# Optimization experiments

Measured on AMD Instinct MI355X. Metric: run time of the kernel, lower is better.

Reference implementation:

```python
import jax, jax.numpy as jnp
import numpy as np

NUM_HEADS = 16
EMBED = 1024
BLOCK = 2048
VOCAB = 32000
HEAD = EMBED // NUM_HEADS


def setup_inputs() -> dict:
    key = jax.random.key(0)
    ks = jax.random.split(key, 9)
    B, T = 2, 2048
    x = jax.random.randint(ks[0], (B, T), 0, VOCAB)
    target = jax.random.randint(ks[1], (B, T), 0, VOCAB)
    s = 0.02
    tok_emb = jax.random.normal(ks[2], (VOCAB, EMBED), jnp.float32) * s
    pos_emb = jax.random.normal(ks[3], (BLOCK, EMBED), jnp.float32) * s
    Wq = jax.random.normal(ks[4], (EMBED, EMBED), jnp.float32) * s
    Wk = jax.random.normal(ks[5], (EMBED, EMBED), jnp.float32) * s
    Wv = jax.random.normal(ks[6], (EMBED, EMBED), jnp.float32) * s
    W_lm = jax.random.normal(ks[7], (EMBED, VOCAB), jnp.float32) * s
    b_lm = jnp.zeros((VOCAB,), jnp.float32)
    return {"x": x, "target": target, "tok_emb": tok_emb, "pos_emb": pos_emb,
            "Wq": Wq, "Wk": Wk, "Wv": Wv, "W_lm": W_lm, "b_lm": b_lm}


def reference(x, target, tok_emb, pos_emb, Wq, Wk, Wv, W_lm, b_lm):
    B, T = x.shape
    h = tok_emb[x] + pos_emb[:T]                       # [B,T,E]
    # fused QKV projections, then split into heads (equivalent to per-head Linears + concat)
    q = (h @ Wq).reshape(B, T, NUM_HEADS, HEAD)
    k = (h @ Wk).reshape(B, T, NUM_HEADS, HEAD)
    v = (h @ Wv).reshape(B, T, NUM_HEADS, HEAD)
    scores = jnp.einsum("bqhd,bkhd->bhqk", q, k) / (HEAD ** 0.5)
    causal = jnp.tril(jnp.ones((T, T), bool))
    scores = jnp.where(causal, scores, -jnp.inf)
    attn = jax.nn.softmax(scores, axis=-1)             # [B,H,T,T]
    out = jnp.einsum("bhqk,bkhd->bqhd", attn, v).reshape(B, T, EMBED)
    logits = out @ W_lm + b_lm                         # [B,T,V]
    logits_flat = logits.reshape(B * T, VOCAB)
    logp = jax.nn.log_softmax(logits_flat, axis=-1)
    loss = -jnp.take_along_axis(logp, target.reshape(-1, 1), axis=-1).mean()
    return logits_flat, loss
```

## Files before the change

kernel.cpp:

```cpp
#include <hip/hip_runtime.h>
#include <cstdint>
#include <cstddef>

#define EMB   1024
#define TSEQ  2048
#define NBATCH 2
#define NHEAD 16
#define HDIM  64
#define VOCAB 32000
#define ROWS  4096
#define NCB   125

typedef __attribute__((ext_vector_type(8))) short short8;
typedef __attribute__((ext_vector_type(4))) float f32x4;

__device__ __forceinline__ unsigned short f2bf(float f) {
  unsigned int u = __float_as_uint(f);
  u = (u + 0x7FFFu + ((u >> 16) & 1u)) >> 16;
  return (unsigned short)u;
}

__device__ __forceinline__ void gload16(const void* g, void* l) {
  typedef __attribute__((address_space(1))) const unsigned int gu;
  typedef __attribute__((address_space(3))) unsigned int lu;
  __builtin_amdgcn_global_load_lds((gu*)g, (lu*)l, 16, 0, 0);
}

__global__ void convT(const float* __restrict__ in, unsigned short* __restrict__ out,
                      int R, int C) {
  __shared__ float tile[32][33];
  const int ct = blockIdx.x, rt = blockIdx.y;
  const int t = threadIdx.x;
  const int r0 = t >> 5;
  const int c  = t & 31;
#pragma unroll
  for (int i = 0; i < 4; ++i) {
    int r = r0 + i * 8;
    tile[r][c] = in[(size_t)(rt * 32 + r) * C + ct * 32 + c];
  }
  __syncthreads();
#pragma unroll
  for (int i = 0; i < 4; ++i) {
    int r = r0 + i * 8;
    out[(size_t)(ct * 32 + r) * R + rt * 32 + c] = f2bf(tile[c][r]);
  }
}

__global__ void embed_kernel(const int* __restrict__ x, const float* __restrict__ tok,
                             const float* __restrict__ pos, unsigned short* __restrict__ h) {
  const int idx = blockIdx.x * 256 + threadIdx.x;
  const int row = idx >> 8;
  const int c4  = idx & 255;
  const int tpos = row & (TSEQ - 1);
  const int token = x[row];
  float4 a = *(const float4*)(tok + (size_t)token * EMB + c4 * 4);
  float4 p = *(const float4*)(pos + (size_t)tpos * EMB + c4 * 4);
  unsigned int lo = (unsigned int)f2bf(a.x + p.x) | ((unsigned int)f2bf(a.y + p.y) << 16);
  unsigned int hi = (unsigned int)f2bf(a.z + p.z) | ((unsigned int)f2bf(a.w + p.w) << 16);
  *(uint2*)(h + (size_t)idx * 4) = make_uint2(lo, hi);
}

template <int EPI>
__global__ void gemm_bt(const unsigned short* __restrict__ A,
                        const unsigned short* __restrict__ Bt,
                        void* __restrict__ Cout,
                        float scale, int M, int N, int K) {
  __shared__ unsigned short As[2][128 * 32];
  __shared__ unsigned short Bs[2][128 * 32];
  const int t  = threadIdx.x;
  const int l  = t & 63;
  const int w  = t >> 6;
  const int wr = w >> 1, wc = w & 1;
  const int m0 = blockIdx.y * 128;
  const int n0 = blockIdx.x * 128;
  const int KT = K >> 5;

  f32x4 acc[4][4] = {};

  const int crow = t >> 2;
  const int coff = (t & 3) * 16;
  const size_t abase = ((size_t)(m0 + crow) * K) * 2 + coff;
  const size_t bbase = ((size_t)(n0 + crow) * K) * 2 + coff;
  const size_t rstep = (size_t)64 * K * 2;
  const char* Ab = (const char*)A;
  const char* Bb = (const char*)Bt;

#define STAGE(buf, kt_) do {                                              \
    size_t ko = (size_t)(kt_) * 64;                                       \
    gload16(Ab + abase + ko,         (char*)&As[(buf)][0] + t * 16);      \
    gload16(Ab + abase + rstep + ko, (char*)&As[(buf)][0] + t * 16 + 4096);\
    gload16(Bb + bbase + ko,         (char*)&Bs[(buf)][0] + t * 16);      \
    gload16(Bb + bbase + rstep + ko, (char*)&Bs[(buf)][0] + t * 16 + 4096);\
  } while (0)

  const int lr  = l & 15;
  const int lkb = (l >> 4) * 16;

#define COMPUTE(buf) do {                                                  \
    const char* ab = (const char*)&As[(buf)][0];                           \
    const char* bb = (const char*)&Bs[(buf)][0];                           \
    short8 fa[4], fb[4];                                                   \
    _Pragma("unroll")                                                      \
    for (int m = 0; m < 4; ++m)                                            \
      fa[m] = *(const short8*)(ab + (wr * 64 + m * 16 + lr) * 64 + lkb);   \
    _Pragma("unroll")                                                      \
    for (int n = 0; n < 4; ++n)                                            \
      fb[n] = *(const short8*)(bb + (wc * 64 + n * 16 + lr) * 64 + lkb);   \
    _Pragma("unroll")                                                      \
    for (int m = 0; m < 4; ++m)                                            \
      _Pragma("unroll")                                                    \
      for (int n = 0; n < 4; ++n)                                          \
        acc[m][n] = __builtin_amdgcn_mfma_f32_16x16x32_bf16(               \
            fa[m], fb[n], acc[m][n], 0, 0, 0);                             \
  } while (0)

  STAGE(0, 0);
  __syncthreads();
  int cur = 0;
  for (int kt = 0; kt < KT; ++kt) {
    if (kt + 1 < KT) STAGE(cur ^ 1, kt + 1);
    COMPUTE(cur);
    __syncthreads();
    cur ^= 1;
  }
#undef STAGE
#undef COMPUTE

  const int orow = m0 + wr * 64 + (l >> 4) * 4;
  const int ocol = n0 + wc * 64 + lr;
#pragma unroll
  for (int m = 0; m < 4; ++m) {
#pragma unroll
    for (int n = 0; n < 4; ++n) {
      const int col = ocol + n * 16;
      if (EPI == 1) {
        unsigned short* C = (unsigned short*)Cout;
#pragma unroll
        for (int r = 0; r < 4; ++r) {
          int row = orow + m * 16 + r;
          C[(size_t)row * N + col] = f2bf(acc[m][n][r] * scale);
        }
      } else {
        unsigned short* C = (unsigned short*)Cout;
        int row0 = orow + m * 16;
        int bb_ = row0 >> 11, tq = row0 & 2047;
        int hh = col >> 6, dd = col & 63;
        unsigned int lo = (unsigned int)f2bf(acc[m][n][0]) | ((unsigned int)f2bf(acc[m][n][1]) << 16);
        unsigned int hi = (unsigned int)f2bf(acc[m][n][2]) | ((unsigned int)f2bf(acc[m][n][3]) << 16);
        *(uint2*)&C[(((size_t)(bb_ * NHEAD + hh) * HDIM + dd) * TSEQ) + tq] = make_uint2(lo, hi);
      }
    }
  }
}

__global__ __launch_bounds__(256)
void attn_mfma(const unsigned short* __restrict__ Qbf,
               const unsigned short* __restrict__ Kbf,
               const unsigned short* __restrict__ Vtbf,
               unsigned short* __restrict__ Obf) {
  const int qt = (gridDim.x - 1) - blockIdx.x;
  const int h  = blockIdx.y;
  const int b  = blockIdx.z;
  const int t  = threadIdx.x, w = t >> 6, l = t & 63;
  const int g  = l >> 4, c = l & 15;
  const int qw = qt * 64 + w * 16;
  const int qg = qw + c;

  __shared__ unsigned short Ks[2][32 * 64];
  __shared__ unsigned short Vs[2][64 * 32];

  const unsigned short* Qrow = Qbf + ((size_t)(b * TSEQ + qg) * EMB + h * HDIM);
  short8 qfrag[2];
  qfrag[0] = *(const short8*)(Qrow + g * 8);
  qfrag[1] = *(const short8*)(Qrow + g * 8 + 32);

  f32x4 accO[4] = {};
  float mrun = -3e38f, lsum = 0.0f;

  const int kvt = t >> 3, kch = t & 7;
  const char* Kg = (const char*)(Kbf + ((size_t)(b * TSEQ + kvt) * EMB + h * HDIM))
                   + (((kch * 16) ^ ((kvt & 7) << 4)));
  const int dt = t >> 2, vch = t & 3;
  const char* Vg = (const char*)(Vtbf + (((size_t)(b * NHEAD + h) * HDIM + dt) * TSEQ))
                   + vch * 16;
  const size_t kstep = (size_t)32 * EMB * 2;
  const size_t vstep = (size_t)32 * 2;

#define ASTAGE(buf, kt_) do {                                               \
    gload16(Kg + (size_t)(kt_) * kstep, (char*)&Ks[buf][0] + t * 16);       \
    gload16(Vg + (size_t)(kt_) * vstep, (char*)&Vs[buf][0] + t * 16);       \
  } while (0)

  const int nkt = 2 * qt + 2;
  ASTAGE(0, 0);
  __syncthreads();
  int cur = 0;
  for (int kt = 0; kt < nkt; ++kt) {
    if (kt + 1 < nkt) ASTAGE(cur ^ 1, kt + 1);
    const int k0 = kt * 32;

    const char* kb = (const char*)&Ks[cur][0];
    f32x4 sa[2] = {};
#pragma unroll
    for (int kc = 0; kc < 2; ++kc) {
#pragma unroll
      for (int kh = 0; kh < 2; ++kh) {
        short8 ka = *(const short8*)(kb + (kc * 16 + c) * 128 +
                                     ((g * 16 + kh * 64) ^ ((c & 7) << 4)));
        sa[kc] = __builtin_amdgcn_mfma_f32_16x16x32_bf16(ka, qfrag[kh], sa[kc], 0, 0, 0);
      }
    }

    float sv[8];
#pragma unroll
    for (int kc = 0; kc < 2; ++kc)
#pragma unroll
      for (int r = 0; r < 4; ++r) {
        int kv = k0 + kc * 16 + g * 4 + r;
        sv[kc * 4 + r] = (kv > qg) ? -3e38f : sa[kc][r];
      }
    float pm = sv[0];
#pragma unroll
    for (int i = 1; i < 8; ++i) pm = fmaxf(pm, sv[i]);
    pm = fmaxf(pm, __shfl_xor(pm, 16));
    pm = fmaxf(pm, __shfl_xor(pm, 32));
    const float mnew = fmaxf(mrun, pm);
    const float alpha = __expf(mrun - mnew);
    float ps = 0.0f;
#pragma unroll
    for (int i = 0; i < 8; ++i) { float p = __expf(sv[i] - mnew); sv[i] = p; ps += p; }
    ps += __shfl_xor(ps, 16);
    ps += __shfl_xor(ps, 32);
    lsum = lsum * alpha + ps;
    mrun = mnew;

#pragma unroll
    for (int r = 0; r < 4; ++r) {
      float ar = __shfl(alpha, g * 4 + r);
      accO[0][r] *= ar; accO[1][r] *= ar; accO[2][r] *= ar; accO[3][r] *= ar;
    }

    unsigned int wf[4];
#pragma unroll
    for (int rp = 0; rp < 2; ++rp)
#pragma unroll
      for (int kc = 0; kc < 2; ++kc) {
        unsigned int rw;
        asm("v_cvt_pk_bf16_f32 %0, %1, %2"
            : "=v"(rw) : "v"(sv[kc * 4 + 2 * rp]), "v"(sv[kc * 4 + 2 * rp + 1]));
        wf[rp * 2 + kc] = rw;
      }

    union { unsigned int u[4]; short8 s8; } pa;
#pragma unroll
    for (int jp = 0; jp < 4; ++jp) {
      int srcLane = c + ((2 * (g & 1) + (jp >> 1)) << 4);
      unsigned int v0 = (unsigned int)__shfl((int)wf[2 * (jp & 1)], srcLane);
      unsigned int v1 = (unsigned int)__shfl((int)wf[2 * (jp & 1) + 1], srcLane);
      pa.u[jp] = (g >> 1) ? v1 : v0;
    }

    const char* vb = (const char*)&Vs[cur][0];
#pragma unroll
    for (int cp = 0; cp < 4; ++cp) {
      short8 vf = *(const short8*)(vb + (c + 16 * cp) * 64 + g * 16);
      accO[cp] = __builtin_amdgcn_mfma_f32_16x16x32_bf16(pa.s8, vf, accO[cp], 0, 0, 0);
    }

    __syncthreads();
    cur ^= 1;
  }
#undef ASTAGE

  const float inv = 1.0f / lsum;
#pragma unroll
  for (int r = 0; r < 4; ++r) {
    float ir = __shfl(inv, g * 4 + r);
    unsigned short* orow = Obf + ((size_t)(b * TSEQ + qw + g * 4 + r) * EMB + h * HDIM);
#pragma unroll
    for (int cp = 0; cp < 4; ++cp)
      orow[c + 16 * cp] = f2bf(accO[cp][r] * ir);
  }
}

__global__ __launch_bounds__(512, 2)
void gemm_lm(const unsigned short* __restrict__ A,
             const unsigned short* __restrict__ Bt,
             const float* __restrict__ bias,
             float* __restrict__ C,
             float* __restrict__ pm, float* __restrict__ ps) {
  extern __shared__ char lds[];
  const int t = threadIdx.x;
  const int w = t >> 6, l = t & 63;
  const int wm = w >> 2, wn = w & 3;
  const int fr = l & 15, kg = l >> 4;

  const int L  = blockIdx.x;
  const int Lp = (L & 7) * 250 + (L >> 3);
  const int mtile = Lp & 15;
  const int ntile = Lp >> 4;

  const char* Ag = (const char*)A;
  const char* Bg = (const char*)Bt;

  const int srow = t >> 3;
  const int scl  = t & 7;
  const int scg  = scl ^ (srow & 7);
  size_t aoff0 = ((size_t)(mtile * 256 +       srow) * EMB) * 2 + scg * 16;
  size_t aoff1 = ((size_t)(mtile * 256 + 128 + srow) * EMB) * 2 + scg * 16;
  size_t boff0 = ((size_t)(ntile * 256 +       srow) * EMB) * 2 + scg * 16;
  size_t boff1 = ((size_t)(ntile * 256 + 128 + srow) * EMB) * 2 + scg * 16;

#define STG_A(buf_, kt_, ah_) do {                                          \
    char* d = lds + (buf_) * 65536 + (ah_) * 16384 + t * 16;                \
    const char* s = Ag + ((ah_) ? aoff1 : aoff0) + (size_t)(kt_) * 128;     \
    gload16(s, d); gload16(s + 131072, d + 8192);                           \
  } while (0)
#define STG_B(buf_, kt_, bh_) do {                                          \
    char* d = lds + (buf_) * 65536 + 32768 + (bh_) * 16384 + t * 16;        \
    const char* s = Bg + ((bh_) ? boff1 : boff0) + (size_t)(kt_) * 128;     \
    gload16(s, d); gload16(s + 131072, d + 8192);                           \
  } while (0)

  const int xr  = fr & 7;
  const int cb0 = (kg ^ xr) * 16;
  const int arow = (wm * 128 + fr) * 128;
  const int brow = (wn * 64 + fr) * 128;

  f32x4 acc[8][4] = {};
  short8 fa[4][2], fb[4][2];

#define MFMA_Q(MH, NH)                                                       \
  _Pragma("unroll")                                                          \
  for (int mi = 0; mi < 4; ++mi)                                             \
    _Pragma("unroll")                                                        \
    for (int ni = 0; ni < 2; ++ni)                                           \
      _Pragma("unroll")                                                      \
      for (int ks = 0; ks < 2; ++ks)                                         \
        acc[(MH)*4+mi][(NH)*2+ni] = __builtin_amdgcn_mfma_f32_16x16x32_bf16( \
            fa[mi][ks], fb[(NH)*2+ni][ks], acc[(MH)*4+mi][(NH)*2+ni], 0,0,0);

#define TILE(h_, S1, S2, VMN) do {                                           \
    const int buf_ = (h_) & 1;                                               \
    char* Abase = lds + buf_ * 65536;                                        \
    char* Bbase = Abase + 32768;                                             \
                                                            \
    _Pragma("unroll")                                                        \
    for (int mi = 0; mi < 4; ++mi) {                                         \
      fa[mi][0] = *(const short8*)(Abase + arow + mi*2048 + cb0);            \
      fa[mi][1] = *(const short8*)(Abase + arow + mi*2048 + (cb0^64));       \
    }                                                                        \
    _Pragma("unroll")                                                        \
    for (int ni = 0; ni < 2; ++ni) {                                         \
      fb[ni][0] = *(const short8*)(Bbase + brow + ni*2048 + cb0);            \
      fb[ni][1] = *(const short8*)(Bbase + brow + ni*2048 + (cb0^64));       \
    }                                                                        \
    if (S1) STG_A(buf_^1, (h_)+1, 0);                                        \
    __builtin_amdgcn_s_barrier();                                            \
    __builtin_amdgcn_s_setprio(1); MFMA_Q(0,0); __builtin_amdgcn_s_setprio(0);\
    __builtin_amdgcn_s_barrier();                                            \
                                                            \
    _Pragma("unroll")                                                        \
    for (int ni = 0; ni < 2; ++ni) {                                         \
      fb[2+ni][0] = *(const short8*)(Bbase + brow + (2+ni)*2048 + cb0);      \
      fb[2+ni][1] = *(const short8*)(Bbase + brow + (2+ni)*2048 + (cb0^64));  \
    }                                                                        \
    if (S1) STG_A(buf_^1, (h_)+1, 1);                                        \
    __builtin_amdgcn_s_barrier();                                            \
    __builtin_amdgcn_s_setprio(1); MFMA_Q(0,1); __builtin_amdgcn_s_setprio(0);\
    __builtin_amdgcn_s_barrier();                                            \
                                                            \
    _Pragma("unroll")                                                        \
    for (int mi = 0; mi < 4; ++mi) {                                         \
      fa[mi][0] = *(const short8*)(Abase + arow + (4+mi)*2048 + cb0);        \
      fa[mi][1] = *(const short8*)(Abase + arow + (4+mi)*2048 + (cb0^64));   \
    }                                                                        \
    if (S2) STG_B(buf_, (h_)+2, 0);                                          \
    __builtin_amdgcn_s_barrier();                                            \
    __builtin_amdgcn_s_setprio(1); MFMA_Q(1,1); __builtin_amdgcn_s_setprio(0);\
    __builtin_amdgcn_s_barrier();                                            \
                                                            \
    if (S2) STG_B(buf_, (h_)+2, 1);                                          \
    __builtin_amdgcn_s_barrier();                                            \
    __builtin_amdgcn_s_setprio(1); MFMA_Q(1,0); __builtin_amdgcn_s_setprio(0);\
    if (VMN) asm volatile("s_waitcnt vmcnt(4)" ::: "memory");                \
    else     asm volatile("s_waitcnt vmcnt(0)" ::: "memory");                \
    __builtin_amdgcn_s_barrier();                                            \
  } while (0)

  STG_B(0, 0, 0); STG_B(0, 0, 1); STG_A(0, 0, 0); STG_A(0, 0, 1);
  STG_B(1, 1, 0); STG_B(1, 1, 1);
  asm volatile("s_waitcnt vmcnt(4)" ::: "memory");
  __builtin_amdgcn_s_barrier();

  for (int h = 0; h < 14; ++h) TILE(h, 1, 1, 4);
  TILE(14, 1, 0, 0);
  TILE(15, 0, 0, 0);
#undef TILE
#undef MFMA_Q
#undef STG_A
#undef STG_B

  __syncthreads();

  const int mrow0 = mtile * 256 + wm * 128;
  const int ncol0 = ntile * 256 + wn * 64;
  float biasv[4];
#pragma unroll
  for (int ni = 0; ni < 4; ++ni) biasv[ni] = bias[ncol0 + ni * 16 + fr];
#pragma unroll
  for (int mi = 0; mi < 8; ++mi)
#pragma unroll
    for (int ni = 0; ni < 4; ++ni)
#pragma unroll
      for (int rr = 0; rr < 4; ++rr)
        acc[mi][ni][rr] += biasv[ni];

#pragma unroll
  for (int mi = 0; mi < 8; ++mi)
#pragma unroll
    for (int rr = 0; rr < 4; ++rr) {
      int row = mrow0 + mi * 16 + kg * 4 + rr;
      float* cr = C + (size_t)row * VOCAB + ncol0 + fr;
#pragma unroll
      for (int ni = 0; ni < 4; ++ni) cr[ni * 16] = acc[mi][ni][rr];
    }

  float* redm = (float*)lds;
  float* reds = (float*)(lds + 4096);
#pragma unroll
  for (int mi = 0; mi < 8; ++mi)
#pragma unroll
    for (int rr = 0; rr < 4; ++rr) {
      float m1 = fmaxf(fmaxf(acc[mi][0][rr], acc[mi][1][rr]),
                       fmaxf(acc[mi][2][rr], acc[mi][3][rr]));
      m1 = fmaxf(m1, __shfl_xor(m1, 1));
      m1 = fmaxf(m1, __shfl_xor(m1, 2));
      m1 = fmaxf(m1, __shfl_xor(m1, 4));
      m1 = fmaxf(m1, __shfl_xor(m1, 8));
      if (fr == 0) redm[(wm * 4 + wn) * 128 + mi * 16 + kg * 4 + rr] = m1;
    }
  __syncthreads();

  float rmx[8][4];
#pragma unroll
  for (int mi = 0; mi < 8; ++mi)
#pragma unroll
    for (int rr = 0; rr < 4; ++rr) {
      int row = mi * 16 + kg * 4 + rr;
      float a0 = fmaxf(redm[(wm*4+0)*128 + row], redm[(wm*4+1)*128 + row]);
      float a1 = fmaxf(redm[(wm*4+2)*128 + row], redm[(wm*4+3)*128 + row]);
      rmx[mi][rr] = fmaxf(a0, a1);
    }
#pragma unroll
  for (int mi = 0; mi < 8; ++mi)
#pragma unroll
    for (int rr = 0; rr < 4; ++rr) {
      float r = rmx[mi][rr];
      float s1 = __expf(acc[mi][0][rr] - r) + __expf(acc[mi][1][rr] - r)
               + __expf(acc[mi][2][rr] - r) + __expf(acc[mi][3][rr] - r);
      s1 += __shfl_xor(s1, 1);
      s1 += __shfl_xor(s1, 2);
      s1 += __shfl_xor(s1, 4);
      s1 += __shfl_xor(s1, 8);
      if (fr == 0) reds[(wm * 4 + wn) * 128 + mi * 16 + kg * 4 + rr] = s1;
    }
  __syncthreads();

  if (wn == 0 && fr == 0) {
#pragma unroll
    for (int mi = 0; mi < 8; ++mi)
#pragma unroll
      for (int rr = 0; rr < 4; ++rr) {
        int row = mi * 16 + kg * 4 + rr;
        float ssum = reds[(wm*4+0)*128 + row] + reds[(wm*4+1)*128 + row]
                   + reds[(wm*4+2)*128 + row] + reds[(wm*4+3)*128 + row];
        int grow = mrow0 + row;
        pm[(size_t)grow * NCB + ntile] = rmx[mi][rr];
        ps[(size_t)grow * NCB + ntile] = ssum;
      }
  }
}

__global__ void loss_rows2(const float* __restrict__ pm, const float* __restrict__ ps,
                           const float* __restrict__ logits, const int* __restrict__ tgt,
                           float* __restrict__ partial) {
  const int row = blockIdx.x * 4 + (threadIdx.x >> 6);
  const int l = threadIdx.x & 63;
  const float* pmr = pm + (size_t)row * NCB;
  const float* psr = ps + (size_t)row * NCB;
  float m = -3e38f, s = 0.0f;
  for (int i = l; i < NCB; i += 64) {
    float mv = pmr[i], sv = psr[i];
    float nm = fmaxf(m, mv);
    s = s * __expf(m - nm) + sv * __expf(mv - nm);
    m = nm;
  }
#pragma unroll
  for (int off = 1; off < 64; off <<= 1) {
    float om = __shfl_xor(m, off), os = __shfl_xor(s, off);
    float nm = fmaxf(m, om);
    s = s * __expf(m - nm) + os * __expf(om - nm);
    m = nm;
  }
  if (l == 0) {
    float lse = m + __logf(s);
    partial[row] = -(logits[(size_t)row * VOCAB + tgt[row]] - lse);
  }
}

__global__ void loss_final(const float* __restrict__ partial, float* __restrict__ out) {
  const int t = threadIdx.x;
  float s = 0.0f;
  for (int i = t; i < ROWS; i += 256) s += partial[i];
#pragma unroll
  for (int off = 1; off < 64; off <<= 1) s += __shfl_xor(s, off);
  __shared__ float ws_[4];
  if ((t & 63) == 0) ws_[t >> 6] = s;
  __syncthreads();
  if (t == 0) out[0] = (ws_[0] + ws_[1] + ws_[2] + ws_[3]) * (1.0f / (float)ROWS);
}

extern "C" void kernel_launch(void* const* d_in, const int* in_sizes, int n_in,
                              void* d_out, int out_size, void* d_ws, size_t ws_size,
                              hipStream_t stream) {
  const int*   x      = (const int*)d_in[0];
  const int*   target = (const int*)d_in[1];
  const float* tok    = (const float*)d_in[2];
  const float* pos    = (const float*)d_in[3];
  const float* Wq     = (const float*)d_in[4];
  const float* Wk     = (const float*)d_in[5];
  const float* Wv     = (const float*)d_in[6];
  const float* Wlm    = (const float*)d_in[7];
  const float* blm    = (const float*)d_in[8];
  float* out = (float*)d_out;

  char* p = (char*)d_ws;
  unsigned short* Wqt  = (unsigned short*)p; p += (size_t)EMB * EMB * 2;
  unsigned short* Wkt  = (unsigned short*)p; p += (size_t)EMB * EMB * 2;
  unsigned short* Wvt  = (unsigned short*)p; p += (size_t)EMB * EMB * 2;
  unsigned short* Wlmt = (unsigned short*)p; p += (size_t)VOCAB * EMB * 2;
  unsigned short* hbf  = (unsigned short*)p; p += (size_t)ROWS * EMB * 2;
  unsigned short* qbf  = (unsigned short*)p; p += (size_t)ROWS * EMB * 2;
  unsigned short* kbf  = (unsigned short*)p; p += (size_t)ROWS * EMB * 2;
  unsigned short* vtbf = (unsigned short*)p; p += (size_t)ROWS * EMB * 2;
  unsigned short* obf  = (unsigned short*)p; p += (size_t)ROWS * EMB * 2;
  float*          prt  = (float*)p;          p += (size_t)ROWS * 4;
  float*          pmw  = (float*)p;          p += (size_t)ROWS * NCB * 4;
  float*          psw  = (float*)p;          p += (size_t)ROWS * NCB * 4;

  hipFuncSetAttribute((const void*)gemm_lm,
                      hipFuncAttributeMaxDynamicSharedMemorySize, 131072);

  dim3 b256(256);
  convT<<<dim3(EMB / 32, EMB / 32), b256, 0, stream>>>(Wq, Wqt, EMB, EMB);
  convT<<<dim3(EMB / 32, EMB / 32), b256, 0, stream>>>(Wk, Wkt, EMB, EMB);
  convT<<<dim3(EMB / 32, EMB / 32), b256, 0, stream>>>(Wv, Wvt, EMB, EMB);
  convT<<<dim3(VOCAB / 32, EMB / 32), b256, 0, stream>>>(Wlm, Wlmt, EMB, VOCAB);

  embed_kernel<<<ROWS * (EMB / 4) / 256, b256, 0, stream>>>(x, tok, pos, hbf);

  gemm_bt<1><<<dim3(EMB / 128, ROWS / 128), b256, 0, stream>>>(hbf, Wqt, qbf, 0.125f, ROWS, EMB, EMB);
  gemm_bt<1><<<dim3(EMB / 128, ROWS / 128), b256, 0, stream>>>(hbf, Wkt, kbf, 1.0f, ROWS, EMB, EMB);
  gemm_bt<2><<<dim3(EMB / 128, ROWS / 128), b256, 0, stream>>>(hbf, Wvt, vtbf, 1.0f, ROWS, EMB, EMB);

  attn_mfma<<<dim3(TSEQ / 64, NHEAD, NBATCH), b256, 0, stream>>>(qbf, kbf, vtbf, obf);

  gemm_lm<<<dim3((ROWS / 256) * (VOCAB / 256)), dim3(512), 131072, stream>>>(
      obf, Wlmt, blm, out, pmw, psw);

  loss_rows2<<<ROWS / 4, b256, 0, stream>>>(pmw, psw, out, target, prt);
  loss_final<<<1, b256, 0, stream>>>(prt, out + (size_t)ROWS * VOCAB);
}
```

Before: 681.4 us.

## Use 1024-thread blocks in LM-head GEMM with smaller per-wave tiles

The LM-head GEMM now runs 16 waves per 256x256 block instead of 8. Each wave owns a 64x64 output sub-tile, so the accumulator and fragment arrays halve, and the staging loads and softmax reduction indexing are re-mapped to match. The pipeline is simplified to two MFMA phases per k-step with fewer barriers. The aim is more waves in flight to hide LDS and global latency, at the cost of more LDS fragment reloads per MFMA and possibly lower occupancy, since only one 128KB-LDS block fits per CU.

```diff
diff --git a/kernel.cpp b/kernel.cpp
--- a/kernel.cpp
+++ b/kernel.cpp
@@ -283,7 +283,7 @@
   }
 }
 
-__global__ __launch_bounds__(512, 2)
+__global__ __launch_bounds__(1024)
 void gemm_lm(const unsigned short* __restrict__ A,
              const unsigned short* __restrict__ Bt,
              const float* __restrict__ bias,
@@ -304,112 +304,93 @@
   const char* Bg = (const char*)Bt;
 
   const int srow = t >> 3;
-  const int scl  = t & 7;
-  const int scg  = scl ^ (srow & 7);
-  size_t aoff0 = ((size_t)(mtile * 256 +       srow) * EMB) * 2 + scg * 16;
-  size_t aoff1 = ((size_t)(mtile * 256 + 128 + srow) * EMB) * 2 + scg * 16;
-  size_t boff0 = ((size_t)(ntile * 256 +       srow) * EMB) * 2 + scg * 16;
-  size_t boff1 = ((size_t)(ntile * 256 + 128 + srow) * EMB) * 2 + scg * 16;
-
-#define STG_A(buf_, kt_, ah_) do {                                          \
-    char* d = lds + (buf_) * 65536 + (ah_) * 16384 + t * 16;                \
-    const char* s = Ag + ((ah_) ? aoff1 : aoff0) + (size_t)(kt_) * 128;     \
-    gload16(s, d); gload16(s + 131072, d + 8192);                           \
+  const int sch  = (t & 7) ^ (srow & 7);
+  const unsigned int aoff0 = ((unsigned int)(mtile * 256 + srow) * EMB) * 2 + sch * 16;
+  const unsigned int boff0 = ((unsigned int)(ntile * 256 + srow) * EMB) * 2 + sch * 16;
+  const int sd = t * 16;
+
+#define STG_A(buf_, kt_) do {                                               \
+    char* d_ = lds + (buf_) * 65536 + sd;                                   \
+    gload16(Ag + aoff0 + (kt_) * 128, d_);                                  \
+    gload16(Ag + aoff0 + 262144u + (kt_) * 128, d_ + 16384);                \
   } while (0)
-#define STG_B(buf_, kt_, bh_) do {                                          \
-    char* d = lds + (buf_) * 65536 + 32768 + (bh_) * 16384 + t * 16;        \
-    const char* s = Bg + ((bh_) ? boff1 : boff0) + (size_t)(kt_) * 128;     \
-    gload16(s, d); gload16(s + 131072, d + 8192);                           \
+#define STG_B(buf_, kt_) do {                                               \
+    char* d_ = lds + (buf_) * 65536 + 32768 + sd;                           \
+    gload16(Bg + boff0 + (kt_) * 128, d_);                                  \
+    gload16(Bg + boff0 + 262144u + (kt_) * 128, d_ + 16384);                \
   } while (0)
 
   const int xr  = fr & 7;
   const int cb0 = (kg ^ xr) * 16;
-  const int arow = (wm * 128 + fr) * 128;
+  const int arow = (wm * 64 + fr) * 128;
   const int brow = (wn * 64 + fr) * 128;
 
-  f32x4 acc[8][4] = {};
-  short8 fa[4][2], fb[4][2];
-
-#define MFMA_Q(MH, NH)                                                       \
+  f32x4 acc[4][4] = {};
+  short8 fa[2][2], fb[4][2];
+
+#define PH_MFMA(MH)                                                          \
   _Pragma("unroll")                                                          \
-  for (int mi = 0; mi < 4; ++mi)                                             \
+  for (int mi = 0; mi < 2; ++mi)                                             \
     _Pragma("unroll")                                                        \
-    for (int ni = 0; ni < 2; ++ni)                                           \
+    for (int ni = 0; ni < 4; ++ni)                                           \
       _Pragma("unroll")                                                      \
       for (int ks = 0; ks < 2; ++ks)                                         \
-        acc[(MH)*4+mi][(NH)*2+ni] = __builtin_amdgcn_mfma_f32_16x16x32_bf16( \
-            fa[mi][ks], fb[(NH)*2+ni][ks], acc[(MH)*4+mi][(NH)*2+ni], 0,0,0);
-
-#define TILE(h_, S1, S2, VMN) do {                                           \
-    const int buf_ = (h_) & 1;                                               \
-    char* Abase = lds + buf_ * 65536;                                        \
-    char* Bbase = Abase + 32768;                                             \
-                                                            \
+        acc[(MH)*2+mi][ni] = __builtin_amdgcn_mfma_f32_16x16x32_bf16(        \
+            fa[mi][ks], fb[ni][ks], acc[(MH)*2+mi][ni], 0, 0, 0);
+
+#define TILE(h_, SA, SB, VMN) do {                                           \
+    const int p_ = (h_) & 1;                                                 \
+    const char* Ab_ = lds + p_ * 65536;                                      \
+    const char* Bb_ = Ab_ + 32768;                                           \
+                                                          \
     _Pragma("unroll")                                                        \
-    for (int mi = 0; mi < 4; ++mi) {                                         \
-      fa[mi][0] = *(const short8*)(Abase + arow + mi*2048 + cb0);            \
-      fa[mi][1] = *(const short8*)(Abase + arow + mi*2048 + (cb0^64));       \
+    for (int mi = 0; mi < 2; ++mi) {                                         \
+      fa[mi][0] = *(const short8*)(Ab_ + arow + mi * 2048 + cb0);            \
+      fa[mi][1] = *(const short8*)(Ab_ + arow + mi * 2048 + (cb0 ^ 64));     \
     }                                                                        \
     _Pragma("unroll")                                                        \
-    for (int ni = 0; ni < 2; ++ni) {                                         \
-      fb[ni][0] = *(const short8*)(Bbase + brow + ni*2048 + cb0);            \
-      fb[ni][1] = *(const short8*)(Bbase + brow + ni*2048 + (cb0^64));       \
+    for (int ni = 0; ni < 4; ++ni) {                                         \
+      fb[ni][0] = *(const short8*)(Bb_ + brow + ni * 2048 + cb0);            \
+      fb[ni][1] = *(const short8*)(Bb_ + brow + ni * 2048 + (cb0 ^ 64));     \
     }                                                                        \
-    if (S1) STG_A(buf_^1, (h_)+1, 0);                                        \
+    if (SA) STG_A(p_ ^ 1, (h_) + 1);                                         \
     __builtin_amdgcn_s_barrier();                                            \
-    __builtin_amdgcn_s_setprio(1); MFMA_Q(0,0); __builtin_amdgcn_s_setprio(0);\
+    __builtin_amdgcn_s_setprio(1); PH_MFMA(0); __builtin_amdgcn_s_setprio(0);\
     __builtin_amdgcn_s_barrier();                                            \
-                                                            \
+                                                          \
     _Pragma("unroll")                                                        \
-    for (int ni = 0; ni < 2; ++ni) {                                         \
-      fb[2+ni][0] = *(const short8*)(Bbase + brow + (2+ni)*2048 + cb0);      \
-      fb[2+ni][1] = *(const short8*)(Bbase + brow + (2+ni)*2048 + (cb0^64));  \
+    for (int mi = 0; mi < 2; ++mi) {                                         \
+      fa[mi][0] = *(const short8*)(Ab_ + arow + (2 + mi) * 2048 + cb0);      \
+      fa[mi][1] = *(const short8*)(Ab_ + arow + (2 + mi) * 2048 + (cb0 ^ 64));\
     }                                                                        \
-    if (S1) STG_A(buf_^1, (h_)+1, 1);                                        \
+    if (SB) STG_B(p_, (h_) + 2);                                             \
     __builtin_amdgcn_s_barrier();                                            \
-    __builtin_amdgcn_s_setprio(1); MFMA_Q(0,1); __builtin_amdgcn_s_setprio(0);\
-    __builtin_amdgcn_s_barrier();                                            \
-                                                            \
-    _Pragma("unroll")                                                        \
-    for (int mi = 0; mi < 4; ++mi) {                                         \
-      fa[mi][0] = *(const short8*)(Abase + arow + (4+mi)*2048 + cb0);        \
-      fa[mi][1] = *(const short8*)(Abase + arow + (4+mi)*2048 + (cb0^64));   \
-    }                                                                        \
-    if (S2) STG_B(buf_, (h_)+2, 0);                                          \
-    __builtin_amdgcn_s_barrier();                                            \
-    __builtin_amdgcn_s_setprio(1); MFMA_Q(1,1); __builtin_amdgcn_s_setprio(0);\
-    __builtin_amdgcn_s_barrier();                                            \
-                                                            \
-    if (S2) STG_B(buf_, (h_)+2, 1);                                          \
-    __builtin_amdgcn_s_barrier();                                            \
-    __builtin_amdgcn_s_setprio(1); MFMA_Q(1,0); __builtin_amdgcn_s_setprio(0);\
-    if (VMN) asm volatile("s_waitcnt vmcnt(4)" ::: "memory");                \
-    else     asm volatile("s_waitcnt vmcnt(0)" ::: "memory");                \
+    __builtin_amdgcn_s_setprio(1); PH_MFMA(1); __builtin_amdgcn_s_setprio(0);\
+    asm volatile("s_waitcnt vmcnt(" #VMN ")" ::: "memory");                  \
     __builtin_amdgcn_s_barrier();                                            \
   } while (0)
 
-  STG_B(0, 0, 0); STG_B(0, 0, 1); STG_A(0, 0, 0); STG_A(0, 0, 1);
-  STG_B(1, 1, 0); STG_B(1, 1, 1);
-  asm volatile("s_waitcnt vmcnt(4)" ::: "memory");
+  STG_A(0, 0); STG_B(0, 0); STG_B(1, 1);
+  asm volatile("s_waitcnt vmcnt(2)" ::: "memory");
   __builtin_amdgcn_s_barrier();
 
-  for (int h = 0; h < 14; ++h) TILE(h, 1, 1, 4);
+  for (int h = 0; h < 14; ++h) TILE(h, 1, 1, 2);
   TILE(14, 1, 0, 0);
   TILE(15, 0, 0, 0);
 #undef TILE
-#undef MFMA_Q
+#undef PH_MFMA
 #undef STG_A
 #undef STG_B
 
   __syncthreads();
 
-  const int mrow0 = mtile * 256 + wm * 128;
+  const int mrow0 = mtile * 256 + wm * 64;
   const int ncol0 = ntile * 256 + wn * 64;
   float biasv[4];
 #pragma unroll
   for (int ni = 0; ni < 4; ++ni) biasv[ni] = bias[ncol0 + ni * 16 + fr];
 #pragma unroll
-  for (int mi = 0; mi < 8; ++mi)
+  for (int mi = 0; mi < 4; ++mi)
 #pragma unroll
     for (int ni = 0; ni < 4; ++ni)
 #pragma unroll
@@ -417,7 +398,7 @@
         acc[mi][ni][rr] += biasv[ni];
 
 #pragma unroll
-  for (int mi = 0; mi < 8; ++mi)
+  for (int mi = 0; mi < 4; ++mi)
 #pragma unroll
     for (int rr = 0; rr < 4; ++rr) {
       int row = mrow0 + mi * 16 + kg * 4 + rr;
@@ -429,7 +410,7 @@
   float* redm = (float*)lds;
   float* reds = (float*)(lds + 4096);
 #pragma unroll
-  for (int mi = 0; mi < 8; ++mi)
+  for (int mi = 0; mi < 4; ++mi)
 #pragma unroll
     for (int rr = 0; rr < 4; ++rr) {
       float m1 = fmaxf(fmaxf(acc[mi][0][rr], acc[mi][1][rr]),
@@ -438,22 +419,22 @@
       m1 = fmaxf(m1, __shfl_xor(m1, 2));
       m1 = fmaxf(m1, __shfl_xor(m1, 4));
       m1 = fmaxf(m1, __shfl_xor(m1, 8));
-      if (fr == 0) redm[(wm * 4 + wn) * 128 + mi * 16 + kg * 4 + rr] = m1;
-    }
-  __syncthreads();
-
-  float rmx[8][4];
-#pragma unroll
-  for (int mi = 0; mi < 8; ++mi)
+      if (fr == 0) redm[wn * 256 + wm * 64 + mi * 16 + kg * 4 + rr] = m1;
+    }
+  __syncthreads();
+
+  float rmx[4][4];
+#pragma unroll
+  for (int mi = 0; mi < 4; ++mi)
 #pragma unroll
     for (int rr = 0; rr < 4; ++rr) {
-      int row = mi * 16 + kg * 4 + rr;
-      float a0 = fmaxf(redm[(wm*4+0)*128 + row], redm[(wm*4+1)*128 + row]);
-      float a1 = fmaxf(redm[(wm*4+2)*128 + row], redm[(wm*4+3)*128 + row]);
+      int row = wm * 64 + mi * 16 + kg * 4 + rr;
+      float a0 = fmaxf(redm[0 * 256 + row], redm[1 * 256 + row]);
+      float a1 = fmaxf(redm[2 * 256 + row], redm[3 * 256 + row]);
       rmx[mi][rr] = fmaxf(a0, a1);
     }
 #pragma unroll
-  for (int mi = 0; mi < 8; ++mi)
+  for (int mi = 0; mi < 4; ++mi)
 #pragma unroll
     for (int rr = 0; rr < 4; ++rr) {
       float r = rmx[mi][rr];
@@ -463,19 +444,19 @@
       s1 += __shfl_xor(s1, 2);
       s1 += __shfl_xor(s1, 4);
       s1 += __shfl_xor(s1, 8);
-      if (fr == 0) reds[(wm * 4 + wn) * 128 + mi * 16 + kg * 4 + rr] = s1;
+      if (fr == 0) reds[wn * 256 + wm * 64 + mi * 16 + kg * 4 + rr] = s1;
     }
   __syncthreads();
 
   if (wn == 0 && fr == 0) {
 #pragma unroll
-    for (int mi = 0; mi < 8; ++mi)
+    for (int mi = 0; mi < 4; ++mi)
 #pragma unroll
       for (int rr = 0; rr < 4; ++rr) {
-        int row = mi * 16 + kg * 4 + rr;
-        float ssum = reds[(wm*4+0)*128 + row] + reds[(wm*4+1)*128 + row]
-                   + reds[(wm*4+2)*128 + row] + reds[(wm*4+3)*128 + row];
-        int grow = mrow0 + row;
+        int row = wm * 64 + mi * 16 + kg * 4 + rr;
+        float ssum = reds[0 * 256 + row] + reds[1 * 256 + row]
+                   + reds[2 * 256 + row] + reds[3 * 256 + row];
+        int grow = mtile * 256 + row;
         pm[(size_t)grow * NCB + ntile] = rmx[mi][rr];
         ps[(size_t)grow * NCB + ntile] = ssum;
       }
@@ -566,7 +547,7 @@
 
   attn_mfma<<<dim3(TSEQ / 64, NHEAD, NBATCH), b256, 0, stream>>>(qbf, kbf, vtbf, obf);
 
-  gemm_lm<<<dim3((ROWS / 256) * (VOCAB / 256)), dim3(512), 131072, stream>>>(
+  gemm_lm<<<dim3((ROWS / 256) * (VOCAB / 256)), dim3(1024), 131072, stream>>>(
       obf, Wlmt, blm, out, pmw, psw);
 
   loss_rows2<<<ROWS / 4, b256, 0, stream>>>(pmw, psw, out, target, prt);
```

After: 711.3 us. 1.04x slower.
